# Optimization experiments

Measured on AMD Instinct MI355X. Metric: run time of the kernel, lower is better.

## Reference

```python
import jax, jax.numpy as jnp
import numpy as np

N, E, H, ED = 50000, 400000, 512, 64
BN_EPS = 1e-5


def setup_inputs() -> dict:
    key = jax.random.key(0)
    ks = jax.random.split(key, 8)
    s = lambda d: 1.0 / np.sqrt(d)
    return {
        "x": jax.random.normal(ks[0], (N, H), jnp.float32),
        "edge_attr": jax.random.normal(ks[1], (E, ED), jnp.float32),
        "edge_index": jax.random.randint(ks[2], (2, E), 0, N, jnp.int32),
        # GINEConv edge projection (edge_dim -> hidden_dim)
        "W_e": jax.random.normal(ks[3], (ED, H), jnp.float32) * s(ED),
        "b_e": jnp.zeros((H,), jnp.float32),
        # 2-layer MLP: Linear(H, 2H) -> BN -> SiLU -> Linear(2H, H)
        "W1": jax.random.normal(ks[4], (H, 2 * H), jnp.float32) * s(H),
        "b1": jnp.zeros((2 * H,), jnp.float32),
        "g1": jnp.ones((2 * H,), jnp.float32),
        "beta1": jnp.zeros((2 * H,), jnp.float32),
        "W2": jax.random.normal(ks[5], (2 * H, H), jnp.float32) * s(2 * H),
        "b2": jnp.zeros((H,), jnp.float32),
        # outer BatchNorm(hidden_dim)
        "g2": jnp.ones((H,), jnp.float32),
        "beta2": jnp.zeros((H,), jnp.float32),
        # trainable GIN epsilon (init 0)
        "eps": jnp.zeros((), jnp.float32),
    }


def _bn(h, g, b):
    # training-mode batch norm over the node dimension (biased variance)
    mu = jnp.mean(h, axis=0)
    var = jnp.mean(jnp.square(h - mu), axis=0)
    return (h - mu) * jax.lax.rsqrt(var + BN_EPS) * g + b


def reference(x, edge_attr, edge_index, W_e, b_e, W1, b1, g1, beta1, W2, b2, g2, beta2, eps):
    src, dst = edge_index[0], edge_index[1]
    # message: ReLU(x_j + lin(e_ij)), gathered per edge  -> [E, H]
    msg = jax.nn.relu(x[src] + edge_attr @ W_e + b_e)
    # scatter-add aggregate into destination nodes -> [N, H]
    aggr = jax.ops.segment_sum(msg, dst, num_segments=x.shape[0])
    # GIN combine + 2-layer MLP with internal BatchNorm + SiLU (dropout=0)
    h = (1.0 + eps) * x + aggr
    h = jax.nn.silu(_bn(h @ W1 + b1, g1, beta1))
    h = h @ W2 + b2
    # outer BatchNorm + SiLU (dropout=0 -> identity)
    return jax.nn.silu(_bn(h, g2, beta2))
```

## Files before the change

### kernel.cpp

```cpp
#include <hip/hip_runtime.h>
#include <math.h>

#define NN 50000
#define NE 400000
#define HD 512
#define EDIM 64
#define H2 1024
#define LDT 72
#define CAP_SLOT 1200000
#define CAP_TILE 75000
#define CAP_HEAVY 8192
#define NBLK_SCAN 98

typedef short s16x8 __attribute__((ext_vector_type(8)));
typedef float f32x4 __attribute__((ext_vector_type(4)));

__device__ __forceinline__ unsigned short f2bf(float f) {
    union { float f; unsigned u; } v; v.f = f;
    unsigned r = v.u + 0x7fffu + ((v.u >> 16) & 1u);
    return (unsigned short)(r >> 16);
}
__device__ __forceinline__ float bf2f(unsigned short h) {
    union { unsigned u; float f; } v; v.u = ((unsigned)h) << 16;
    return v.f;
}
__device__ __forceinline__ float silu_f(float t) {
    return t / (1.f + __expf(-t));
}
__device__ __forceinline__ void gload_lds16(const unsigned short* g, unsigned short* l) {
    __builtin_amdgcn_global_load_lds(
        (const __attribute__((address_space(1))) unsigned int*)(g),
        (__attribute__((address_space(3))) unsigned int*)(l), 16, 0, 0);
}

constexpr size_t OFF_AGGRC = 0;
constexpr size_t OFF_XB   = 16777216;
constexpr size_t OFF_H1   = 0;
constexpr size_t OFF_H    = 102400000;
constexpr size_t OFF_WET  = 153600000;
constexpr size_t OFF_W1T  = OFF_WET + 65536;
constexpr size_t OFF_W2T  = OFF_W1T + 1048576;
constexpr size_t OFF_CNT  = OFF_W2T + 1048576;
constexpr size_t OFF_B1S  = OFF_CNT + 200000;
constexpr size_t OFF_B1Q  = OFF_B1S + 4096;
constexpr size_t OFF_B2S  = OFF_B1Q + 4096;
constexpr size_t OFF_B2Q  = OFF_B2S + 2048;
constexpr size_t ZERO_BYTES = 200000 + 4096 + 4096 + 2048 + 2048;
constexpr size_t OFF_TEX  = OFF_B2Q + 2048;
constexpr size_t OFF_BSUM = OFF_TEX + 200000;
constexpr size_t OFF_BOFF = OFF_BSUM + 512;
constexpr size_t OFF_T    = OFF_BOFF + 512;
constexpr size_t OFF_CUR  = OFF_T + 64;
constexpr size_t OFF_NOT  = OFF_CUR + 200000;
constexpr size_t OFF_SRCP = OFF_NOT + 300032;
constexpr size_t OFF_EIXP = OFF_SRCP + 4800000;
constexpr size_t OFF_SC1  = OFF_EIXP + 4800000;
constexpr size_t OFF_SB1  = OFF_SC1 + 4096;
constexpr size_t OFF_SC2  = OFF_SB1 + 4096;
constexpr size_t OFF_SB2  = OFF_SC2 + 2048;

__global__ __launch_bounds__(256) void k_convert(const float* __restrict__ We,
    const float* __restrict__ W1, const float* __restrict__ W2,
    unsigned short* __restrict__ wet, unsigned short* __restrict__ w1t,
    unsigned short* __restrict__ w2t) {
    int i = blockIdx.x * 256 + threadIdx.x;
    if (i < 32768) {
        int n = i >> 6, k = i & 63;
        wet[i] = f2bf(We[k * HD + n]);
    } else if (i < 32768 + 524288) {
        int j = i - 32768;
        int n = j >> 9, k = j & 511;
        w1t[j] = f2bf(W1[k * H2 + n]);
    } else if (i < 32768 + 2 * 524288) {
        int j = i - (32768 + 524288);
        int n = j >> 10, k = j & 1023;
        w2t[j] = f2bf(W2[k * HD + n]);
    }
}

__global__ __launch_bounds__(256) void k_xconv(const float* __restrict__ x,
    unsigned short* __restrict__ xb) {
    int t = blockIdx.x * 256 + threadIdx.x;
    if (t >= NN * 64) return;
    int n = t >> 6, rem = t & 63;
    int cb = rem >> 4, l = rem & 15;
    const float* src = x + (size_t)n * HD + cb * 128 + l;
    unsigned short o[8];
    #pragma unroll
    for (int j = 0; j < 8; ++j) o[j] = f2bf(src[j * 16]);
    *(uint4*)(xb + (size_t)n * HD + cb * 128 + l * 8) = *(const uint4*)o;
}

__global__ __launch_bounds__(256) void k_hist(const int* __restrict__ dst, int* __restrict__ counts) {
    int e = blockIdx.x * 256 + threadIdx.x;
    if (e < NE) atomicAdd(&counts[dst[e]], 1);
}

__global__ __launch_bounds__(512) void k_scan1(const int* __restrict__ counts,
    int* __restrict__ tile_excl, int* __restrict__ bsum) {
    __shared__ int wsums[8];
    int b = blockIdx.x, t = threadIdx.x;
    int i = b * 512 + t;
    int v = (i < NN) ? ((counts[i] + 15) >> 4) : 0;
    int lane = t & 63, wid = t >> 6;
    int x = v;
    #pragma unroll
    for (int o = 1; o < 64; o <<= 1) {
        int y = __shfl_up(x, o, 64);
        if (lane >= o) x += y;
    }
    if (lane == 63) wsums[wid] = x;
    __syncthreads();
    if (t == 0) {
        int run = 0;
        for (int w = 0; w < 8; ++w) { int tmp = wsums[w]; wsums[w] = run; run += tmp; }
    }
    __syncthreads();
    int excl = x - v + wsums[wid];
    if (i < NN) tile_excl[i] = excl;
    if (t == 511) bsum[b] = excl + v;
}

__global__ void k_scan2(const int* __restrict__ bsum, int* __restrict__ boff, int* __restrict__ Tout) {
    if (threadIdx.x == 0) {
        int run = 0;
        for (int b = 0; b < NBLK_SCAN; ++b) { boff[b] = run; run += bsum[b]; }
        Tout[0] = run;
        Tout[1] = 0;
    }
}

__global__ __launch_bounds__(512) void k_scan3(const int* __restrict__ counts,
    int* __restrict__ tile_excl, const int* __restrict__ boff,
    int* __restrict__ cursor, int* __restrict__ node_of_tile, int* __restrict__ Tout) {
    int b = blockIdx.x, t = threadIdx.x;
    int i = b * 512 + t;
    if (i >= NN) return;
    int tc = (counts[i] + 15) >> 4;
    int ts = tile_excl[i] + boff[b];
    cursor[i] = ts * 16;
    int hid = -1;
    if (tc > 1) {
        hid = atomicAdd(&Tout[1], 1);
        if (hid >= CAP_HEAVY) hid = CAP_HEAVY - 1;
    }
    tile_excl[i] = hid;
    unsigned tag = (tc > 1) ? (0x80000000u | (unsigned)hid) : (unsigned)i;
    for (int k = 0; k < tc; ++k) node_of_tile[ts + k] = (int)tag;
}

__global__ __launch_bounds__(256) void k_scatter(const int* __restrict__ src, const int* __restrict__ dst,
    int* __restrict__ cursor, int* __restrict__ srcp, int* __restrict__ eidxp) {
    int e = blockIdx.x * 256 + threadIdx.x;
    if (e < NE) {
        int d = dst[e];
        int p = atomicAdd(&cursor[d], 1);
        srcp[p] = src[e];
        eidxp[p] = e;
    }
}

__global__ __launch_bounds__(256, 4) void k_edge(
    const float* __restrict__ ea, const unsigned short* __restrict__ wet,
    const unsigned short* __restrict__ xb, const float* __restrict__ b_e,
    const float* __restrict__ eps,
    const int* __restrict__ srcp, const int* __restrict__ eidxp,
    const int* __restrict__ node_of_tile, const int* __restrict__ Tptr,
    float* __restrict__ aggrc, unsigned short* __restrict__ h) {
    int tile0 = blockIdx.x * 2;
    int T = Tptr[0];
    if (tile0 >= T) return;
    __shared__ unsigned short As[32 * LDT];
    __shared__ int Ss[32];
    __shared__ float Rs[4][128];
    int t = threadIdx.x;
    int slot0 = tile0 * 16;
    {
        int r = t >> 3, qq = t & 7;
        int s = srcp[slot0 + r];
        if (qq == 0) Ss[r] = s;
        unsigned short* lp = As + r * LDT + qq * 8;
        if (s >= 0) {
            int eix = eidxp[slot0 + r];
            const float* gp = ea + (size_t)eix * EDIM + qq * 8;
            float4 v0 = ((const float4*)gp)[0];
            float4 v1 = ((const float4*)gp)[1];
            lp[0] = f2bf(v0.x); lp[1] = f2bf(v0.y); lp[2] = f2bf(v0.z); lp[3] = f2bf(v0.w);
            lp[4] = f2bf(v1.x); lp[5] = f2bf(v1.y); lp[6] = f2bf(v1.z); lp[7] = f2bf(v1.w);
        } else {
            uint4 z = {0u, 0u, 0u, 0u};
            *(uint4*)lp = z;
        }
    }
    __syncthreads();
    int wave = t >> 6, lane = t & 63, l15 = lane & 15, quad = lane >> 4;
    int cblk = wave * 128;
    f32x4 acc[2][8];
    #pragma unroll
    for (int i = 0; i < 2; ++i)
        #pragma unroll
        for (int j = 0; j < 8; ++j) acc[i][j] = (f32x4){0.f, 0.f, 0.f, 0.f};
    #pragma unroll
    for (int k0 = 0; k0 < 64; k0 += 32) {
        s16x8 af[2], bfr[8];
        #pragma unroll
        for (int i = 0; i < 2; ++i)
            af[i] = *(const s16x8*)(As + (i * 16 + l15) * LDT + k0 + quad * 8);
        #pragma unroll
        for (int j = 0; j < 8; ++j)
            bfr[j] = *(const s16x8*)(wet + (size_t)(cblk + j * 16 + l15) * EDIM + k0 + quad * 8);
        #pragma unroll
        for (int i = 0; i < 2; ++i)
            #pragma unroll
            for (int j = 0; j < 8; ++j)
                acc[i][j] = __builtin_amdgcn_mfma_f32_16x16x32_bf16(af[i], bfr[j], acc[i][j], 0, 0, 0);
    }
    float ep = 1.0f + eps[0];
    float bev[8];
    #pragma unroll
    for (int j = 0; j < 8; ++j) bev[j] = b_e[cblk + j * 16 + l15];
    float* rp = Rs[wave];
    #pragma unroll
    for (int i = 0; i < 2; ++i) {
        int tile = tile0 + i;
        unsigned meta = (unsigned)node_of_tile[tile];
        int v = (int)(meta & 0x7fffffffu);
        int vc = v < NN ? v : 0;
        int srow = i * 16 + quad * 4;
        s16x8 xr[4]; float msk[4];
        #pragma unroll
        for (int r = 0; r < 4; ++r) {
            int s = Ss[srow + r];
            msk[r] = s >= 0 ? 1.f : 0.f;
            xr[r] = *(const s16x8*)(xb + (size_t)(s >= 0 ? s : 0) * HD + cblk + l15 * 8);
        }
        s16x8 xo = *(const s16x8*)(xb + (size_t)vc * HD + cblk + l15 * 8);
        float sum8[8];
        #pragma unroll
        for (int j = 0; j < 8; ++j) sum8[j] = 0.f;
        #pragma unroll
        for (int r = 0; r < 4; ++r) {
            #pragma unroll
            for (int j = 0; j < 8; ++j) {
                float vv = acc[i][j][r] + bf2f((unsigned short)xr[r][j]) + bev[j];
                vv = vv > 0.f ? vv : 0.f;
                sum8[j] = fmaf(msk[r], vv, sum8[j]);
            }
        }
        #pragma unroll
        for (int j = 0; j < 8; ++j) {
            sum8[j] += __shfl_xor(sum8[j], 16, 64);
            sum8[j] += __shfl_xor(sum8[j], 32, 64);
        }
        if (tile < T) {
            if (meta & 0x80000000u) {
                if (quad == 0) {
                    float* ap = aggrc + (size_t)v * HD + cblk;
                    #pragma unroll
                    for (int j = 0; j < 8; ++j) atomicAdd(ap + j * 16 + l15, sum8[j]);
                }
            } else {
                int j0 = quad * 2, j1 = j0 + 1;
                rp[j0 * 16 + l15] = fmaf(ep, bf2f((unsigned short)xo[j0]), sum8[j0]);
                rp[j1 * 16 + l15] = fmaf(ep, bf2f((unsigned short)xo[j1]), sum8[j1]);
                unsigned pk = (unsigned)f2bf(rp[lane * 2]) |
                              ((unsigned)f2bf(rp[lane * 2 + 1]) << 16);
                *(unsigned*)(h + (size_t)v * HD + cblk + lane * 2) = pk;
            }
        }
    }
}

__global__ __launch_bounds__(256) void k_combine_heavy(const float* __restrict__ aggrc,
    const float* __restrict__ x, const int* __restrict__ counts, const int* __restrict__ hidmap,
    const float* __restrict__ eps, unsigned short* __restrict__ h) {
    long i = ((long)blockIdx.x * 256 + threadIdx.x) * 4;
    if (i >= (long)NN * HD) return;
    int v = (int)(i >> 9);
    int c = counts[v];
    if (c >= 1 && c <= 16) return;
    float ep = 1.0f + eps[0];
    float4 a = {0.f, 0.f, 0.f, 0.f};
    if (c > 16) a = *(const float4*)(aggrc + (size_t)hidmap[v] * HD + (i & (HD - 1)));
    float4 xv = *(const float4*)(x + i);
    uint2 p;
    p.x = (unsigned)f2bf(ep * xv.x + a.x) | ((unsigned)f2bf(ep * xv.y + a.y) << 16);
    p.y = (unsigned)f2bf(ep * xv.z + a.z) | ((unsigned)f2bf(ep * xv.w + a.w) << 16);
    *(uint2*)(h + i) = p;
}

template <bool BF16OUT, bool SILU_A>
__global__ __launch_bounds__(256) void k_gemm_bn(
    const unsigned short* __restrict__ A, const unsigned short* __restrict__ Bt,
    const float* __restrict__ bias, void* __restrict__ Cv,
    float* __restrict__ bn_sum, float* __restrict__ bn_sumsq,
    const float* __restrict__ a_sc, const float* __restrict__ a_sb,
    int M, int K, int Nn) {
    __shared__ unsigned short As[SILU_A ? (64 * LDT) : (64 * 64)];
    __shared__ unsigned short Bs[128 * 64];
    __shared__ float csum[128], csumsq[128];
    constexpr int LDA = SILU_A ? LDT : 64;
    int nwg = gridDim.x;
    int q = nwg >> 3, r = nwg & 7;
    int xk = blockIdx.x & 7, xj = blockIdx.x >> 3;
    int logical = xk * q + (xk < r ? xk : r) + xj;
    int nnb = Nn >> 7;
    int mblk = logical / nnb, nblk = logical - mblk * nnb;
    int t = threadIdx.x;
    int row0 = mblk * 64, col0 = nblk * 128;
    int wid = t >> 6, lane = t & 63, l15 = lane & 15, quad = lane >> 4;
    int wr = wid >> 1, wc = wid & 1;
    int rb = (lane >> 3), cb8 = (lane & 7) * 8;
    int scb8 = cb8 ^ (rb * 8);
    int rswz = (l15 & 7) * 8;
    f32x4 acc[2][4];
    #pragma unroll
    for (int i = 0; i < 2; ++i)
        #pragma unroll
        for (int j = 0; j < 4; ++j) acc[i][j] = (f32x4){0.f, 0.f, 0.f, 0.f};

    for (int k0 = 0; k0 < K; k0 += 64) {
        __syncthreads();
        #pragma unroll
        for (int c = 0; c < 4; ++c) {
            int row = (wid * 4 + c) * 8 + rb;
            gload_lds16(Bt + (size_t)(col0 + row) * K + k0 + scb8,
                        Bs + row * 64 + cb8);
        }
        if constexpr (!SILU_A) {
            #pragma unroll
            for (int c = 0; c < 2; ++c) {
                int row = (wid * 2 + c) * 8 + rb;
                gload_lds16(A + (size_t)(row0 + row) * K + k0 + scb8,
                            As + row * 64 + cb8);
            }
        } else {
            int rr = t >> 2, qtr = t & 3;
            int row = row0 + rr;
            int kb = k0 + qtr * 16;
            unsigned short* lp = As + rr * LDT + qtr * 16;
            if (row < M) {
                const unsigned short* gp = A + (size_t)row * K + kb;
                #pragma unroll
                for (int jj = 0; jj < 2; ++jj) {
                    uint4 u = *(const uint4*)(gp + jj * 8);
                    float4 sA = *(const float4*)(a_sc + kb + jj * 8);
                    float4 sB = *(const float4*)(a_sc + kb + jj * 8 + 4);
                    float4 bA = *(const float4*)(a_sb + kb + jj * 8);
                    float4 bB = *(const float4*)(a_sb + kb + jj * 8 + 4);
                    unsigned short o[8];
                    o[0] = f2bf(silu_f(bf2f((unsigned short)(u.x & 0xffffu)) * sA.x + bA.x));
                    o[1] = f2bf(silu_f(bf2f((unsigned short)(u.x >> 16)) * sA.y + bA.y));
                    o[2] = f2bf(silu_f(bf2f((unsigned short)(u.y & 0xffffu)) * sA.z + bA.z));
                    o[3] = f2bf(silu_f(bf2f((unsigned short)(u.y >> 16)) * sA.w + bA.w));
                    o[4] = f2bf(silu_f(bf2f((unsigned short)(u.z & 0xffffu)) * sB.x + bB.x));
                    o[5] = f2bf(silu_f(bf2f((unsigned short)(u.z >> 16)) * sB.y + bB.y));
                    o[6] = f2bf(silu_f(bf2f((unsigned short)(u.w & 0xffffu)) * sB.z + bB.z));
                    o[7] = f2bf(silu_f(bf2f((unsigned short)(u.w >> 16)) * sB.w + bB.w));
                    #pragma unroll
                    for (int m = 0; m < 8; ++m) lp[jj * 8 + m] = o[m];
                }
            } else {
                uint4 z = {0u, 0u, 0u, 0u};
                *(uint4*)(lp) = z;
                *(uint4*)(lp + 8) = z;
            }
        }
        __syncthreads();
        #pragma unroll
        for (int kk = 0; kk < 64; kk += 32) {
            s16x8 af[2], bfr[4];
            #pragma unroll
            for (int i = 0; i < 2; ++i) {
                if constexpr (SILU_A)
                    af[i] = *(const s16x8*)(As + (wr * 32 + i * 16 + l15) * LDA + kk + quad * 8);
                else
                    af[i] = *(const s16x8*)(As + (wr * 32 + i * 16 + l15) * 64 + ((kk + quad * 8) ^ rswz));
            }
            #pragma unroll
            for (int j = 0; j < 4; ++j)
                bfr[j] = *(const s16x8*)(Bs + (wc * 64 + j * 16 + l15) * 64 + ((kk + quad * 8) ^ rswz));
            #pragma unroll
            for (int i = 0; i < 2; ++i)
                #pragma unroll
                for (int j = 0; j < 4; ++j)
                    acc[i][j] = __builtin_amdgcn_mfma_f32_16x16x32_bf16(af[i], bfr[j], acc[i][j], 0, 0, 0);
        }
    }
    if (t < 128) { csum[t] = 0.f; csumsq[t] = 0.f; }
    __syncthreads();
    int mrow0 = row0 + wr * 32;
    #pragma unroll
    for (int j = 0; j < 4; ++j) {
        int col = wc * 64 + j * 16 + l15;
        float bv = bias[col0 + col];
        float ls = 0.f, lq = 0.f;
        #pragma unroll
        for (int i = 0; i < 2; ++i) {
            #pragma unroll
            for (int r2 = 0; r2 < 4; ++r2) {
                int row = mrow0 + i * 16 + quad * 4 + r2;
                if (row < M) {
                    float v = acc[i][j][r2] + bv;
                    if (BF16OUT)
                        ((unsigned short*)Cv)[(size_t)row * Nn + col0 + col] = f2bf(v);
                    else
                        ((float*)Cv)[(size_t)row * Nn + col0 + col] = v;
                    ls += v; lq += v * v;
                }
            }
        }
        ls += __shfl_xor(ls, 16, 64); ls += __shfl_xor(ls, 32, 64);
        lq += __shfl_xor(lq, 16, 64); lq += __shfl_xor(lq, 32, 64);
        if (quad == 0) {
            atomicAdd(&csum[col], ls);
            atomicAdd(&csumsq[col], lq);
        }
    }
    __syncthreads();
    if (t < 128) {
        atomicAdd(bn_sum + col0 + t, csum[t]);
        atomicAdd(bn_sumsq + col0 + t, csumsq[t]);
    }
}

__global__ __launch_bounds__(256) void k_bn_final(const float* __restrict__ s,
    const float* __restrict__ q, const float* __restrict__ g, const float* __restrict__ beta,
    float* __restrict__ scale, float* __restrict__ sbias, int C, float invN) {
    int c = blockIdx.x * 256 + threadIdx.x;
    if (c < C) {
        float mu = s[c] * invN;
        float var = q[c] * invN - mu * mu;
        var = fmaxf(var, 0.f);
        float sc = g[c] * rsqrtf(var + 1e-5f);
        scale[c] = sc;
        sbias[c] = beta[c] - mu * sc;
    }
}

__global__ __launch_bounds__(256) void k_out(float* __restrict__ out,
    const float* __restrict__ sc, const float* __restrict__ sb, long total) {
    long i = ((long)blockIdx.x * 256 + threadIdx.x) * 4;
    if (i >= total) return;
    int c = (int)(i & (HD - 1));
    float4 v = *(const float4*)(out + i);
    float4 s4 = *(const float4*)(sc + c);
    float4 b4 = *(const float4*)(sb + c);
    float4 o;
    o.x = silu_f(v.x * s4.x + b4.x);
    o.y = silu_f(v.y * s4.y + b4.y);
    o.z = silu_f(v.z * s4.z + b4.z);
    o.w = silu_f(v.w * s4.w + b4.w);
    *(float4*)(out + i) = o;
}

extern "C" void kernel_launch(void* const* d_in, const int* in_sizes, int n_in,
                              void* d_out, int out_size, void* d_ws, size_t ws_size,
                              hipStream_t stream) {
    const float* x      = (const float*)d_in[0];
    const float* ea     = (const float*)d_in[1];
    const int*   ei     = (const int*)d_in[2];
    const float* W_e    = (const float*)d_in[3];
    const float* b_e    = (const float*)d_in[4];
    const float* W1     = (const float*)d_in[5];
    const float* b1     = (const float*)d_in[6];
    const float* g1     = (const float*)d_in[7];
    const float* beta1  = (const float*)d_in[8];
    const float* W2     = (const float*)d_in[9];
    const float* b2     = (const float*)d_in[10];
    const float* g2     = (const float*)d_in[11];
    const float* beta2  = (const float*)d_in[12];
    const float* eps    = (const float*)d_in[13];
    float* out = (float*)d_out;
    char* ws = (char*)d_ws;

    float*          aggrc = (float*)(ws + OFF_AGGRC);
    unsigned short* xb   = (unsigned short*)(ws + OFF_XB);
    unsigned short* h1   = (unsigned short*)(ws + OFF_H1);
    unsigned short* h    = (unsigned short*)(ws + OFF_H);
    unsigned short* wet  = (unsigned short*)(ws + OFF_WET);
    unsigned short* w1t  = (unsigned short*)(ws + OFF_W1T);
    unsigned short* w2t  = (unsigned short*)(ws + OFF_W2T);
    int* counts  = (int*)(ws + OFF_CNT);
    float* b1s   = (float*)(ws + OFF_B1S);
    float* b1q   = (float*)(ws + OFF_B1Q);
    float* b2s   = (float*)(ws + OFF_B2S);
    float* b2q   = (float*)(ws + OFF_B2Q);
    int* tex     = (int*)(ws + OFF_TEX);
    int* bsum    = (int*)(ws + OFF_BSUM);
    int* boff    = (int*)(ws + OFF_BOFF);
    int* Tptr    = (int*)(ws + OFF_T);
    int* cursor  = (int*)(ws + OFF_CUR);
    int* notile  = (int*)(ws + OFF_NOT);
    int* srcp    = (int*)(ws + OFF_SRCP);
    int* eidxp   = (int*)(ws + OFF_EIXP);
    float* sc1   = (float*)(ws + OFF_SC1);
    float* sb1   = (float*)(ws + OFF_SB1);
    float* sc2   = (float*)(ws + OFF_SC2);
    float* sb2   = (float*)(ws + OFF_SB2);

    hipMemsetAsync(aggrc, 0, (size_t)CAP_HEAVY * HD * 4, stream);
    hipMemsetAsync(ws + OFF_CNT, 0, ZERO_BYTES, stream);
    hipMemsetAsync(srcp, 0xFF, (size_t)CAP_SLOT * 4, stream);
    k_convert<<<4224, 256, 0, stream>>>(W_e, W1, W2, wet, w1t, w2t);
    k_xconv<<<(NN * 64 + 255) / 256, 256, 0, stream>>>(x, xb);
    k_hist<<<(NE + 255) / 256, 256, 0, stream>>>(ei + NE, counts);
    k_scan1<<<NBLK_SCAN, 512, 0, stream>>>(counts, tex, bsum);
    k_scan2<<<1, 64, 0, stream>>>(bsum, boff, Tptr);
    k_scan3<<<NBLK_SCAN, 512, 0, stream>>>(counts, tex, boff, cursor, notile, Tptr);
    k_scatter<<<(NE + 255) / 256, 256, 0, stream>>>(ei, ei + NE, cursor, srcp, eidxp);
    k_edge<<<CAP_TILE / 2, 256, 0, stream>>>(ea, wet, xb, b_e, eps, srcp, eidxp, notile, Tptr, aggrc, h);
    k_combine_heavy<<<(int)(((long)NN * HD / 4 + 255) / 256), 256, 0, stream>>>(
        aggrc, x, counts, tex, eps, h);
    k_gemm_bn<true, false><<<((NN + 63) / 64) * (H2 / 128), 256, 0, stream>>>(
        h, w1t, b1, h1, b1s, b1q, nullptr, nullptr, NN, HD, H2);
    k_bn_final<<<4, 256, 0, stream>>>(b1s, b1q, g1, beta1, sc1, sb1, H2, 1.f / NN);
    k_gemm_bn<false, true><<<((NN + 63) / 64) * (HD / 128), 256, 0, stream>>>(
        h1, w2t, b2, out, b2s, b2q, sc1, sb1, NN, H2, HD);
    k_bn_final<<<2, 256, 0, stream>>>(b2s, b2q, g2, beta2, sc2, sb2, HD, 1.f / NN);
    k_out<<<(int)(((long)NN * HD / 4 + 255) / 256), 256, 0, stream>>>(out, sc2, sb2, (long)NN * HD);
}
```

Measured before the change: 883.4 us.

## Pack two low-degree nodes per 16-edge tile to cut padded edge work

Nodes with 1 to 8 incoming edges now share a 16-slot tile in half-tiles of 8 slots. The scan packs full-tile and half-tile counts into one integer, and node_of_tile encodes either a node pair or a single or heavy node. k_edge reduces over only half the quads for paired tiles and writes two nodes' rows. With an average degree of 8, this roughly halves the padded tiles and the edge GEMM and gather work, at the cost of more complex metadata and branching.

After: 836.2 us, median of 2. 5.3% less time.

```diff
diff --git a/kernel.cpp b/kernel.cpp
--- a/kernel.cpp
+++ b/kernel.cpp
@@ -101,7 +101,10 @@
     __shared__ int wsums[8];
     int b = blockIdx.x, t = threadIdx.x;
     int i = b * 512 + t;
-    int v = (i < NN) ? ((counts[i] + 15) >> 4) : 0;
+    int c = (i < NN) ? counts[i] : 0;
+    int v = 0;
+    if (c > 8) v = (c + 15) >> 4;
+    else if (c >= 1) v = 0x10000;
     int lane = t & 63, wid = t >> 6;
     int x = v;
     #pragma unroll
@@ -121,32 +124,50 @@
     if (t == 511) bsum[b] = excl + v;
 }
 
-__global__ void k_scan2(const int* __restrict__ bsum, int* __restrict__ boff, int* __restrict__ Tout) {
+__global__ void k_scan2(int* __restrict__ bsum, int* __restrict__ boff, int* __restrict__ Tout) {
     if (threadIdx.x == 0) {
-        int run = 0;
-        for (int b = 0; b < NBLK_SCAN; ++b) { boff[b] = run; run += bsum[b]; }
-        Tout[0] = run;
+        int runf = 0, runh = 0;
+        for (int b = 0; b < NBLK_SCAN; ++b) {
+            int pk = bsum[b];
+            boff[b] = runf;
+            bsum[b] = runh;
+            runf += pk & 0xFFFF;
+            runh += pk >> 16;
+        }
+        Tout[0] = runf;
         Tout[1] = 0;
+        Tout[2] = runh;
     }
 }
 
 __global__ __launch_bounds__(512) void k_scan3(const int* __restrict__ counts,
-    int* __restrict__ tile_excl, const int* __restrict__ boff,
+    int* __restrict__ tile_excl, const int* __restrict__ boff, const int* __restrict__ bsum,
     int* __restrict__ cursor, int* __restrict__ node_of_tile, int* __restrict__ Tout) {
     int b = blockIdx.x, t = threadIdx.x;
     int i = b * 512 + t;
     if (i >= NN) return;
-    int tc = (counts[i] + 15) >> 4;
-    int ts = tile_excl[i] + boff[b];
-    cursor[i] = ts * 16;
+    int c = counts[i];
+    int pk = tile_excl[i];
     int hid = -1;
-    if (tc > 1) {
-        hid = atomicAdd(&Tout[1], 1);
-        if (hid >= CAP_HEAVY) hid = CAP_HEAVY - 1;
+    if (c >= 1 && c <= 8) {
+        int halfidx = (pk >> 16) + bsum[b];
+        int tile = Tout[0] + (halfidx >> 1);
+        cursor[i] = tile * 16 + (halfidx & 1) * 8;
+        ((unsigned short*)node_of_tile)[tile * 2 + (halfidx & 1)] = (unsigned short)i;
+    } else if (c > 8) {
+        int tc = (c + 15) >> 4;
+        int ts = (pk & 0xFFFF) + boff[b];
+        cursor[i] = ts * 16;
+        if (c <= 16) {
+            node_of_tile[ts] = (int)(0xFFFF0000u | (unsigned)i);
+        } else {
+            hid = atomicAdd(&Tout[1], 1);
+            if (hid >= CAP_HEAVY) hid = CAP_HEAVY - 1;
+            for (int k = 0; k < tc; ++k)
+                node_of_tile[ts + k] = (int)(0xFFFE0000u | (unsigned)hid);
+        }
     }
     tile_excl[i] = hid;
-    unsigned tag = (tc > 1) ? (0x80000000u | (unsigned)hid) : (unsigned)i;
-    for (int k = 0; k < tc; ++k) node_of_tile[ts + k] = (int)tag;
 }
 
 __global__ __launch_bounds__(256) void k_scatter(const int* __restrict__ src, const int* __restrict__ dst,
@@ -168,11 +189,11 @@
     const int* __restrict__ node_of_tile, const int* __restrict__ Tptr,
     float* __restrict__ aggrc, unsigned short* __restrict__ h) {
     int tile0 = blockIdx.x * 2;
-    int T = Tptr[0];
+    int T = Tptr[0] + ((Tptr[2] + 1) >> 1);
     if (tile0 >= T) return;
     __shared__ unsigned short As[32 * LDT];
     __shared__ int Ss[32];
-    __shared__ float Rs[4][128];
+    __shared__ float Rs[4][256];
     int t = threadIdx.x;
     int slot0 = tile0 * 16;
     {
@@ -224,8 +245,10 @@
     for (int i = 0; i < 2; ++i) {
         int tile = tile0 + i;
         unsigned meta = (unsigned)node_of_tile[tile];
-        int v = (int)(meta & 0x7fffffffu);
-        int vc = v < NN ? v : 0;
+        unsigned idA = meta & 0xFFFFu, idB = meta >> 16;
+        bool pair = idB < 0xFFFEu;
+        int v_own = pair ? (quad < 2 ? (int)idA : (int)idB) : (int)idA;
+        int vc = v_own < NN ? v_own : 0;
         int srow = i * 16 + quad * 4;
         s16x8 xr[4]; float msk[4];
         #pragma unroll
@@ -248,24 +271,41 @@
             }
         }
         #pragma unroll
-        for (int j = 0; j < 8; ++j) {
-            sum8[j] += __shfl_xor(sum8[j], 16, 64);
-            sum8[j] += __shfl_xor(sum8[j], 32, 64);
-        }
+        for (int j = 0; j < 8; ++j) sum8[j] += __shfl_xor(sum8[j], 16, 64);
         if (tile < T) {
-            if (meta & 0x80000000u) {
-                if (quad == 0) {
-                    float* ap = aggrc + (size_t)v * HD + cblk;
-                    #pragma unroll
-                    for (int j = 0; j < 8; ++j) atomicAdd(ap + j * 16 + l15, sum8[j]);
+            if (pair) {
+                #pragma unroll
+                for (int j = 0; j < 8; ++j) {
+                    float val = fmaf(ep, bf2f((unsigned short)xo[j]), sum8[j]);
+                    if (quad == 0) rp[j * 16 + l15] = val;
+                    if (quad == 2) rp[128 + j * 16 + l15] = val;
                 }
+                __builtin_amdgcn_sched_barrier(0);
+                int l2 = lane & 31;
+                const float* rb_ = rp + (lane >> 5) * 128 + l2 * 4;
+                float4 v4 = *(const float4*)rb_;
+                uint2 pk;
+                pk.x = (unsigned)f2bf(v4.x) | ((unsigned)f2bf(v4.y) << 16);
+                pk.y = (unsigned)f2bf(v4.z) | ((unsigned)f2bf(v4.w) << 16);
+                *(uint2*)(h + (size_t)v_own * HD + cblk + l2 * 4) = pk;
             } else {
-                int j0 = quad * 2, j1 = j0 + 1;
-                rp[j0 * 16 + l15] = fmaf(ep, bf2f((unsigned short)xo[j0]), sum8[j0]);
-                rp[j1 * 16 + l15] = fmaf(ep, bf2f((unsigned short)xo[j1]), sum8[j1]);
-                unsigned pk = (unsigned)f2bf(rp[lane * 2]) |
-                              ((unsigned)f2bf(rp[lane * 2 + 1]) << 16);
-                *(unsigned*)(h + (size_t)v * HD + cblk + lane * 2) = pk;
+                #pragma unroll
+                for (int j = 0; j < 8; ++j) sum8[j] += __shfl_xor(sum8[j], 32, 64);
+                if (idB == 0xFFFEu) {
+                    if (quad == 0) {
+                        float* ap = aggrc + (size_t)idA * HD + cblk;
+                        #pragma unroll
+                        for (int j = 0; j < 8; ++j) atomicAdd(ap + j * 16 + l15, sum8[j]);
+                    }
+                } else {
+                    int j0 = quad * 2, j1 = j0 + 1;
+                    rp[j0 * 16 + l15] = fmaf(ep, bf2f((unsigned short)xo[j0]), sum8[j0]);
+                    rp[j1 * 16 + l15] = fmaf(ep, bf2f((unsigned short)xo[j1]), sum8[j1]);
+                    __builtin_amdgcn_sched_barrier(0);
+                    unsigned pk = (unsigned)f2bf(rp[lane * 2]) |
+                                  ((unsigned)f2bf(rp[lane * 2 + 1]) << 16);
+                    *(unsigned*)(h + (size_t)idA * HD + cblk + lane * 2) = pk;
+                }
             }
         }
     }
@@ -501,13 +541,14 @@
 
     hipMemsetAsync(aggrc, 0, (size_t)CAP_HEAVY * HD * 4, stream);
     hipMemsetAsync(ws + OFF_CNT, 0, ZERO_BYTES, stream);
+    hipMemsetAsync(notile, 0xFF, 300032, stream);
     hipMemsetAsync(srcp, 0xFF, (size_t)CAP_SLOT * 4, stream);
     k_convert<<<4224, 256, 0, stream>>>(W_e, W1, W2, wet, w1t, w2t);
     k_xconv<<<(NN * 64 + 255) / 256, 256, 0, stream>>>(x, xb);
     k_hist<<<(NE + 255) / 256, 256, 0, stream>>>(ei + NE, counts);
     k_scan1<<<NBLK_SCAN, 512, 0, stream>>>(counts, tex, bsum);
     k_scan2<<<1, 64, 0, stream>>>(bsum, boff, Tptr);
-    k_scan3<<<NBLK_SCAN, 512, 0, stream>>>(counts, tex, boff, cursor, notile, Tptr);
+    k_scan3<<<NBLK_SCAN, 512, 0, stream>>>(counts, tex, boff, bsum, cursor, notile, Tptr);
     k_scatter<<<(NE + 255) / 256, 256, 0, stream>>>(ei, ei + NE, cursor, srcp, eidxp);
     k_edge<<<CAP_TILE / 2, 256, 0, stream>>>(ea, wet, xb, b_e, eps, srcp, eidxp, notile, Tptr, aggrc, h);
     k_combine_heavy<<<(int)(((long)NN * HD / 4 + 255) / 256), 256, 0, stream>>>(
```
